# Kernel optimization log

Hardware: AMD Instinct MI355X
Metric: run time of the kernel (lower is better)

The kernel has to match this reference:

```python
import jax, jax.numpy as jnp
import numpy as np

T, B, IN, H = 1024, 128, 256, 512


def setup_inputs() -> dict:
    key = jax.random.key(0)
    k1, k2, k3, k4, k5 = jax.random.split(key, 5)
    s = 1.0 / np.sqrt(H)  # PyTorch LSTM init scale
    return {
        "x": jax.random.normal(k1, (T, B, IN), dtype=jnp.float32),
        "W_ih": jax.random.normal(k2, (4 * H, IN), dtype=jnp.float32) * s,
        "W_hh": jax.random.normal(k3, (4 * H, H), dtype=jnp.float32) * s,
        "b_ih": jax.random.normal(k4, (4 * H,), dtype=jnp.float32) * s,
        "b_hh": jax.random.normal(k5, (4 * H,), dtype=jnp.float32) * s,
    }


def reference(x, W_ih, W_hh, b_ih, b_hh):
    # Single-layer unidirectional LSTM scanned over the full sequence.
    # PyTorch gate order within the 4H dim: i, f, g, o.
    b = b_ih + b_hh
    Wx = jnp.einsum('tbi,gi->tbg', x, W_ih) + b  # precompute input projection [T,B,4H]

    def step(carry, zx):
        h, c = carry
        z = zx + h @ W_hh.T  # [B, 4H]
        i, f, g, o = jnp.split(z, 4, axis=-1)
        i = jax.nn.sigmoid(i)
        f = jax.nn.sigmoid(f)
        g = jnp.tanh(g)
        o = jax.nn.sigmoid(o)
        c = f * c + i * g
        h = o * jnp.tanh(c)
        return (h, c), None

    h0 = jnp.zeros((B, H), dtype=x.dtype)
    c0 = jnp.zeros((B, H), dtype=x.dtype)
    (h, c), _ = jax.lax.scan(step, (h0, c0), Wx)
    # Original returns the LAST step's output plus (h_n, c_n); with 1 layer output == h_n.
    output = h[None]          # [1, B, H]
    h_n = h[None]             # [num_layers=1, B, H]
    c_n = c[None]
    return (output, h_n, c_n)
```

## Files before the change

kernel.cpp:

```cpp
#include <hip/hip_runtime.h>
#include <hip/hip_bf16.h>

typedef __attribute__((ext_vector_type(8)))  short short8;
typedef __attribute__((ext_vector_type(16))) float f32x16;
typedef __attribute__((ext_vector_type(4)))  unsigned int uint4v;

#define TSTEPS 1024
#define BATCH  128
#define NIN    256
#define NHID   512
#define GM     4
#define MBLK   32
#define XPSTR  528
#define XBUF   8448
#define HSTR   520
#define HBUF   16640

__device__ __forceinline__ unsigned short f2bf(float f) {
  unsigned int u = __builtin_bit_cast(unsigned int, f);
  u += 0x7fffu + ((u >> 16) & 1u);
  return (unsigned short)(u >> 16);
}

__device__ __forceinline__ unsigned long long pack4(float a, float b, float c, float d) {
  return (unsigned long long)f2bf(a)
       | ((unsigned long long)f2bf(b) << 16)
       | ((unsigned long long)f2bf(c) << 32)
       | ((unsigned long long)f2bf(d) << 48);
}

__device__ __forceinline__ float sigf(float x) {
  return 1.0f / (1.0f + __expf(-x));
}
__device__ __forceinline__ float tanh_fast(float x) {
  x = fminf(fmaxf(x, -15.0f), 15.0f);
  float e = __expf(2.0f * x);
  return (e - 1.0f) / (e + 1.0f);
}

__global__ void init_ws_kernel(unsigned long long* hbuf, unsigned int* flags) {
  int idx = blockIdx.x * blockDim.x + threadIdx.x;
  if (idx < 16384) hbuf[idx] = 0ull;
  if (idx < 8192) flags[idx] = 0u;
}

__global__ void convert_x_kernel(const float* __restrict__ x, unsigned short* __restrict__ xbf) {
  const int N4 = TSTEPS * BATCH * NIN / 4;
  for (int i = blockIdx.x * blockDim.x + threadIdx.x; i < N4; i += gridDim.x * blockDim.x) {
    float4 f = *(const float4*)(x + (size_t)i * 4);
    *(unsigned long long*)(xbf + (size_t)i * 4) = pack4(f.x, f.y, f.z, f.w);
  }
}

#define MFMA(va, fb, acc) \
  acc = __builtin_amdgcn_mfma_f32_32x32x16_bf16(va, fb, acc, 0, 0, 0)

template <int USE_DMA>
__global__ __launch_bounds__(256, 1) void lstm_persistent(
    const float* __restrict__ x,
    const unsigned short* __restrict__ xbf,
    const float* __restrict__ Wih,
    const float* __restrict__ Whh,
    const float* __restrict__ bih,
    const float* __restrict__ bhh,
    float* __restrict__ out,
    unsigned long long* __restrict__ hbuf,
    unsigned int* __restrict__ flags)
{
  const int tid  = threadIdx.x;
  const int lane = tid & 63;
  const int wv   = tid >> 6;
  const int gm   = blockIdx.x & (GM - 1);
  const int gh   = blockIdx.x >> 2;
  const int m0   = gm * MBLK;
  const int hc0  = gh * 32;

  __shared__ short x_flat[3 * XBUF];
  __shared__ short h_flat[2 * HBUF];
  __shared__ float z_lds[4][MBLK][36];

  const int ncol = lane & 31;
  const int h5   = lane >> 5;
  const int arow = lane & 31;
  const int kg   = h5 * 8;
  const int gate = ncol >> 3;
  const int wrow = gate * NHID + hc0 + wv * 8 + (ncol & 7);

  short8 bfrag[48];
#pragma unroll
  for (int kb = 0; kb < 48; ++kb) {
    const float* src = (kb < 16)
        ? (Wih + (size_t)wrow * NIN  + (kb * 16 + kg))
        : (Whh + (size_t)wrow * NHID + (kb * 16 + kg - NIN));
    float4 f0 = *(const float4*)src;
    float4 f1 = *(const float4*)(src + 4);
    short8 b;
    b[0] = (short)f2bf(f0.x); b[1] = (short)f2bf(f0.y);
    b[2] = (short)f2bf(f0.z); b[3] = (short)f2bf(f0.w);
    b[4] = (short)f2bf(f1.x); b[5] = (short)f2bf(f1.y);
    b[6] = (short)f2bf(f1.z); b[7] = (short)f2bf(f1.w);
    bfrag[kb] = b;
  }
  const float bias_c = bih[wrow] + bhh[wrow];

  const int grow = tid >> 3;
  const int c4   = (tid & 7) * 4;
  float creg[4] = {0.0f, 0.0f, 0.0f, 0.0f};

  unsigned int* fgrp   = flags + gm * (64 * 32);
  unsigned int* myflag = fgrp + (gh * 4 + wv) * 32;

#define XLOAD(i, v) { int u = tid + 256 * (i); \
    v = *(const float4*)(xt + (size_t)(u >> 6) * NIN + (u & 63) * 4); }
#define XPACK(bb, i, v) { int u = tid + 256 * (i); int r = u >> 6; int hc = u & 63; \
    *(unsigned long long*)&x_flat[(bb) * XBUF + (r >> 1) * XPSTR + (r & 1) * NIN + hc * 4] \
        = pack4(v.x, v.y, v.z, v.w); }
#define XDMA(tt, bb) { \
    const unsigned short* gsrc = xbf + ((size_t)(tt) * BATCH + m0) * NIN; \
    short* ldst = x_flat + (bb) * XBUF; \
    _Pragma("unroll") \
    for (int j = 0; j < 4; ++j) { \
      int ck = 4 * wv + j; \
      const unsigned short* gp = gsrc + (size_t)(2 * ck + h5) * NIN + (lane & 31) * 8; \
      __builtin_amdgcn_global_load_lds((const unsigned int*)gp, \
          (unsigned int*)(ldst + ck * XPSTR), 16, 0, 0); \
    } }

  f32x16 a0, a1, a2, a3;
  float4 xv0, xv1, xv2, xv3, xv4, xv5, xv6, xv7;

  if (USE_DMA) {
    XDMA(0, 0) XDMA(1, 1) XDMA(2, 2)
    asm volatile("s_waitcnt vmcnt(0)" ::: "memory");
  } else {
    { const float* xt = x + (size_t)m0 * NIN;
      XLOAD(0, xv0) XLOAD(1, xv1) XLOAD(2, xv2) XLOAD(3, xv3)
      XLOAD(4, xv4) XLOAD(5, xv5) XLOAD(6, xv6) XLOAD(7, xv7)
      XPACK(0, 0, xv0) XPACK(0, 1, xv1) XPACK(0, 2, xv2) XPACK(0, 3, xv3)
      XPACK(0, 4, xv4) XPACK(0, 5, xv5) XPACK(0, 6, xv6) XPACK(0, 7, xv7) }
    { const float* xt = x + ((size_t)BATCH + m0) * NIN;
      XLOAD(0, xv0) XLOAD(1, xv1) XLOAD(2, xv2) XLOAD(3, xv3)
      XLOAD(4, xv4) XLOAD(5, xv5) XLOAD(6, xv6) XLOAD(7, xv7)
      XPACK(1, 0, xv0) XPACK(1, 1, xv1) XPACK(1, 2, xv2) XPACK(1, 3, xv3)
      XPACK(1, 4, xv4) XPACK(1, 5, xv5) XPACK(1, 6, xv6) XPACK(1, 7, xv7) }
  }
  __syncthreads();
  a0 = (f32x16)bias_c; a1 = (f32x16)0.0f; a2 = (f32x16)0.0f; a3 = (f32x16)0.0f;
  {
    const short* xrow = x_flat + (arow >> 1) * XPSTR + (arow & 1) * NIN + kg;
#pragma unroll
    for (int kb = 0; kb < 16; kb += 4) {
      MFMA(*(const short8*)(xrow + (kb + 0) * 16), bfrag[kb + 0], a0);
      MFMA(*(const short8*)(xrow + (kb + 1) * 16), bfrag[kb + 1], a1);
      MFMA(*(const short8*)(xrow + (kb + 2) * 16), bfrag[kb + 2], a2);
      MFMA(*(const short8*)(xrow + (kb + 3) * 16), bfrag[kb + 3], a3);
    }
  }

  int tmod = 0;
  for (int t = 0; t < TSTEPS; ++t) {
    if (t > 0) {
      const unsigned int* fp = fgrp + lane * 32;
      unsigned int v = __hip_atomic_load(fp, __ATOMIC_RELAXED, __HIP_MEMORY_SCOPE_AGENT);
      while (!__all((int)(v >= (unsigned int)t))) {
        v = __hip_atomic_load(fp, __ATOMIC_RELAXED, __HIP_MEMORY_SCOPE_AGENT);
      }
    }

    {
      const char* p =
          (const char*)(hbuf + (size_t)(t & 1) * 16384 + (size_t)m0 * 128) + tid * 16;
      uint4v hv0, hv1, hv2, hv3, hv4, hv5, hv6, hv7;
      asm volatile("global_load_dwordx4 %0, %1, off sc0 sc1" : "=v"(hv0) : "v"(p + 0 * 4096));
      asm volatile("global_load_dwordx4 %0, %1, off sc0 sc1" : "=v"(hv1) : "v"(p + 1 * 4096));
      asm volatile("global_load_dwordx4 %0, %1, off sc0 sc1" : "=v"(hv2) : "v"(p + 2 * 4096));
      asm volatile("global_load_dwordx4 %0, %1, off sc0 sc1" : "=v"(hv3) : "v"(p + 3 * 4096));
      asm volatile("global_load_dwordx4 %0, %1, off sc0 sc1" : "=v"(hv4) : "v"(p + 4 * 4096));
      asm volatile("global_load_dwordx4 %0, %1, off sc0 sc1" : "=v"(hv5) : "v"(p + 5 * 4096));
      asm volatile("global_load_dwordx4 %0, %1, off sc0 sc1" : "=v"(hv6) : "v"(p + 6 * 4096));
      asm volatile("global_load_dwordx4 %0, %1, off sc0 sc1" : "=v"(hv7) : "v"(p + 7 * 4096));
      asm volatile("s_waitcnt vmcnt(0)" ::: "memory");
      __builtin_amdgcn_sched_barrier(0);
      short* hdst = h_flat + (t & 1) * HBUF;
#pragma unroll
      for (int i = 0; i < 8; ++i) {
        int r = wv + 4 * i;
        uint4v v = (i == 0) ? hv0 : (i == 1) ? hv1 : (i == 2) ? hv2 : (i == 3) ? hv3
                 : (i == 4) ? hv4 : (i == 5) ? hv5 : (i == 6) ? hv6 : hv7;
        *(uint4v*)&hdst[r * HSTR + lane * 8] = v;
      }
    }
    __syncthreads();

    if (!USE_DMA && t + 2 < TSTEPS) {
      const float* xt = x + ((size_t)(t + 2) * BATCH + m0) * NIN;
      XLOAD(0, xv0) XLOAD(1, xv1) XLOAD(2, xv2) XLOAD(3, xv3)
      XLOAD(4, xv4) XLOAD(5, xv5) XLOAD(6, xv6) XLOAD(7, xv7)
    }

    {
      const short* hrow = h_flat + (t & 1) * HBUF + arow * HSTR + kg;
#pragma unroll
      for (int kb = 0; kb < 32; kb += 4) {
        MFMA(*(const short8*)(hrow + (kb + 0) * 16), bfrag[16 + kb + 0], a0);
        MFMA(*(const short8*)(hrow + (kb + 1) * 16), bfrag[16 + kb + 1], a1);
        MFMA(*(const short8*)(hrow + (kb + 2) * 16), bfrag[16 + kb + 2], a2);
        MFMA(*(const short8*)(hrow + (kb + 3) * 16), bfrag[16 + kb + 3], a3);
      }
    }

    {
      f32x16 acc = (a0 + a1) + (a2 + a3);
#pragma unroll
      for (int r = 0; r < 16; ++r) {
        int zr = (r & 3) + 8 * (r >> 2) + 4 * h5;
        z_lds[wv][zr][ncol] = acc[r];
      }
    }
    __syncthreads();

    {
      const int wz = c4 >> 3;
      const int cc = c4 & 7;
      const float* zrow = &z_lds[wz][grow][0];
      float4 vi = *(const float4*)&zrow[ 0 + cc];
      float4 vf = *(const float4*)&zrow[ 8 + cc];
      float4 vg = *(const float4*)&zrow[16 + cc];
      float4 vo = *(const float4*)&zrow[24 + cc];
      float zi[4] = {vi.x, vi.y, vi.z, vi.w};
      float zf[4] = {vf.x, vf.y, vf.z, vf.w};
      float zg[4] = {vg.x, vg.y, vg.z, vg.w};
      float zo[4] = {vo.x, vo.y, vo.z, vo.w};
      float hnv[4];
#pragma unroll
      for (int u = 0; u < 4; ++u) {
        float iv = sigf(zi[u]);
        float fv = sigf(zf[u]);
        float gv = tanh_fast(zg[u]);
        float ov = sigf(zo[u]);
        float cn = fv * creg[u] + iv * gv;
        creg[u] = cn;
        hnv[u] = ov * tanh_fast(cn);
      }
      if (t == TSTEPS - 1) {
        size_t o = (size_t)(m0 + grow) * NHID + hc0 + c4;
        float4 hq; hq.x = hnv[0]; hq.y = hnv[1]; hq.z = hnv[2]; hq.w = hnv[3];
        float4 cq; cq.x = creg[0]; cq.y = creg[1]; cq.z = creg[2]; cq.w = creg[3];
        *(float4*)&out[o]          = hq;
        *(float4*)&out[65536 + o]  = hq;
        *(float4*)&out[131072 + o] = cq;
      } else {
        unsigned long long hp = pack4(hnv[0], hnv[1], hnv[2], hnv[3]);
        size_t hoff = (size_t)((t + 1) & 1) * 16384
                    + (size_t)(m0 + grow) * 128 + (hc0 + c4) / 4;
        __hip_atomic_store(hbuf + hoff, hp, __ATOMIC_RELAXED, __HIP_MEMORY_SCOPE_AGENT);
        __builtin_amdgcn_sched_barrier(0);
        asm volatile("s_waitcnt vmcnt(0)" ::: "memory");
        if (lane == 0) {
          __hip_atomic_store(myflag, (unsigned int)(t + 1),
                             __ATOMIC_RELAXED, __HIP_MEMORY_SCOPE_AGENT);
        }
      }
    }

    if (t < TSTEPS - 1) {
      if (USE_DMA) {
        if (t + 3 < TSTEPS) { XDMA(t + 3, tmod) }
      } else if (t + 2 < TSTEPS) {
        int pb = tmod + 2; if (pb >= 3) pb -= 3;
        XPACK(pb, 0, xv0) XPACK(pb, 1, xv1) XPACK(pb, 2, xv2) XPACK(pb, 3, xv3)
        XPACK(pb, 4, xv4) XPACK(pb, 5, xv5) XPACK(pb, 6, xv6) XPACK(pb, 7, xv7)
      }
      int nb = tmod + 1; if (nb >= 3) nb -= 3;
      a0 = (f32x16)bias_c; a1 = (f32x16)0.0f; a2 = (f32x16)0.0f; a3 = (f32x16)0.0f;
      const short* xrow = x_flat + nb * XBUF + (arow >> 1) * XPSTR + (arow & 1) * NIN + kg;
#pragma unroll
      for (int kb = 0; kb < 16; kb += 4) {
        MFMA(*(const short8*)(xrow + (kb + 0) * 16), bfrag[kb + 0], a0);
        MFMA(*(const short8*)(xrow + (kb + 1) * 16), bfrag[kb + 1], a1);
        MFMA(*(const short8*)(xrow + (kb + 2) * 16), bfrag[kb + 2], a2);
        MFMA(*(const short8*)(xrow + (kb + 3) * 16), bfrag[kb + 3], a3);
      }
    }
    tmod = tmod + 1; if (tmod >= 3) tmod = 0;
  }
#undef XLOAD
#undef XPACK
#undef XDMA
}

extern "C" void kernel_launch(void* const* d_in, const int* in_sizes, int n_in,
                              void* d_out, int out_size, void* d_ws, size_t ws_size,
                              hipStream_t stream) {
  const float* x   = (const float*)d_in[0];
  const float* Wih = (const float*)d_in[1];
  const float* Whh = (const float*)d_in[2];
  const float* bih = (const float*)d_in[3];
  const float* bhh = (const float*)d_in[4];
  float* out = (float*)d_out;

  unsigned long long* hbuf = (unsigned long long*)d_ws;
  unsigned int* flags = (unsigned int*)((char*)d_ws + 262144);
  unsigned short* xbf = (unsigned short*)((char*)d_ws + (1 << 20));

  size_t need = (size_t)(1 << 20) + (size_t)TSTEPS * BATCH * NIN * 2;
  bool dma = ws_size >= need;

  hipLaunchKernelGGL(init_ws_kernel, dim3(64), dim3(256), 0, stream, hbuf, flags);
  if (dma) {
    hipLaunchKernelGGL(convert_x_kernel, dim3(8192), dim3(256), 0, stream, x, xbf);
    hipLaunchKernelGGL((lstm_persistent<1>), dim3(64), dim3(256), 0, stream,
                       x, xbf, Wih, Whh, bih, bhh, out, hbuf, flags);
  } else {
    hipLaunchKernelGGL((lstm_persistent<0>), dim3(64), dim3(256), 0, stream,
                       x, xbf, Wih, Whh, bih, bhh, out, hbuf, flags);
  }
}
```

Measured before the change: 3.565 ms.

## Embed step tags in hidden-state records to replace separate flag polling

Each 8-byte bf16 hidden-state chunk is now written as a 16-byte record with the timestep tag alongside it, in a single store. Consumers poll the records themselves until every tag matches the current step, which removes the separate flag spin-wait and the store-then-wait-then-flag round trip on the serial critical path. In exchange, it doubles the bytes moved per step for hidden-state exchange. It also relies on each 16-byte store being observed atomically, so data and tag arrive together.

```diff
diff --git a/kernel.cpp b/kernel.cpp
--- a/kernel.cpp
+++ b/kernel.cpp
@@ -38,10 +38,9 @@
   return (e - 1.0f) / (e + 1.0f);
 }
 
-__global__ void init_ws_kernel(unsigned long long* hbuf, unsigned int* flags) {
+__global__ void init_ws_kernel(unsigned long long* tbuf) {
   int idx = blockIdx.x * blockDim.x + threadIdx.x;
-  if (idx < 16384) hbuf[idx] = 0ull;
-  if (idx < 8192) flags[idx] = 0u;
+  for (int i = idx; i < 65536; i += 16384) tbuf[i] = 0ull;
 }
 
 __global__ void convert_x_kernel(const float* __restrict__ x, unsigned short* __restrict__ xbf) {
@@ -54,6 +53,9 @@
 
 #define MFMA(va, fb, acc) \
   acc = __builtin_amdgcn_mfma_f32_32x32x16_bf16(va, fb, acc, 0, 0, 0)
+
+#define CLOAD(cv, off) \
+  asm volatile("global_load_dwordx4 %0, %1, off sc0 sc1" : "=v"(cv) : "v"(rb + (off)))
 
 template <int USE_DMA>
 __global__ __launch_bounds__(256, 1) void lstm_persistent(
@@ -64,8 +66,7 @@
     const float* __restrict__ bih,
     const float* __restrict__ bhh,
     float* __restrict__ out,
-    unsigned long long* __restrict__ hbuf,
-    unsigned int* __restrict__ flags)
+    char* __restrict__ tbuf)
 {
   const int tid  = threadIdx.x;
   const int lane = tid & 63;
@@ -107,8 +108,8 @@
   const int c4   = (tid & 7) * 4;
   float creg[4] = {0.0f, 0.0f, 0.0f, 0.0f};
 
-  unsigned int* fgrp   = flags + gm * (64 * 32);
-  unsigned int* myflag = fgrp + (gh * 4 + wv) * 32;
+  const char* tb = tbuf + (size_t)gm * 131072;
+  const int  myci = grow * 128 + (hc0 >> 2) + (tid & 7);
 
 #define XLOAD(i, v) { int u = tid + 256 * (i); \
     v = *(const float4*)(xt + (size_t)(u >> 6) * NIN + (u & 63) * 4); }
@@ -159,36 +160,34 @@
 
   int tmod = 0;
   for (int t = 0; t < TSTEPS; ++t) {
-    if (t > 0) {
-      const unsigned int* fp = fgrp + lane * 32;
-      unsigned int v = __hip_atomic_load(fp, __ATOMIC_RELAXED, __HIP_MEMORY_SCOPE_AGENT);
-      while (!__all((int)(v >= (unsigned int)t))) {
-        v = __hip_atomic_load(fp, __ATOMIC_RELAXED, __HIP_MEMORY_SCOPE_AGENT);
-      }
-    }
-
     {
-      const char* p =
-          (const char*)(hbuf + (size_t)(t & 1) * 16384 + (size_t)m0 * 128) + tid * 16;
-      uint4v hv0, hv1, hv2, hv3, hv4, hv5, hv6, hv7;
-      asm volatile("global_load_dwordx4 %0, %1, off sc0 sc1" : "=v"(hv0) : "v"(p + 0 * 4096));
-      asm volatile("global_load_dwordx4 %0, %1, off sc0 sc1" : "=v"(hv1) : "v"(p + 1 * 4096));
-      asm volatile("global_load_dwordx4 %0, %1, off sc0 sc1" : "=v"(hv2) : "v"(p + 2 * 4096));
-      asm volatile("global_load_dwordx4 %0, %1, off sc0 sc1" : "=v"(hv3) : "v"(p + 3 * 4096));
-      asm volatile("global_load_dwordx4 %0, %1, off sc0 sc1" : "=v"(hv4) : "v"(p + 4 * 4096));
-      asm volatile("global_load_dwordx4 %0, %1, off sc0 sc1" : "=v"(hv5) : "v"(p + 5 * 4096));
-      asm volatile("global_load_dwordx4 %0, %1, off sc0 sc1" : "=v"(hv6) : "v"(p + 6 * 4096));
-      asm volatile("global_load_dwordx4 %0, %1, off sc0 sc1" : "=v"(hv7) : "v"(p + 7 * 4096));
-      asm volatile("s_waitcnt vmcnt(0)" ::: "memory");
+      const char* rb = tb + (size_t)(t & 1) * 65536 + (size_t)tid * 16;
+      const unsigned int tg = (unsigned int)t;
+      uint4v c0, c1, c2, c3, c4v, c5, c6, c7, c8, c9, c10, c11, c12, c13, c14, c15;
+      int ok;
+      do {
+        CLOAD(c0,  0 * 4096); CLOAD(c1,  1 * 4096); CLOAD(c2,  2 * 4096);
+        CLOAD(c3,  3 * 4096); CLOAD(c4v, 4 * 4096); CLOAD(c5,  5 * 4096);
+        CLOAD(c6,  6 * 4096); CLOAD(c7,  7 * 4096); CLOAD(c8,  8 * 4096);
+        CLOAD(c9,  9 * 4096); CLOAD(c10, 10 * 4096); CLOAD(c11, 11 * 4096);
+        CLOAD(c12, 12 * 4096); CLOAD(c13, 13 * 4096); CLOAD(c14, 14 * 4096);
+        CLOAD(c15, 15 * 4096);
+        asm volatile("s_waitcnt vmcnt(0)" ::: "memory");
+        ok = (c0.z == tg) & (c1.z == tg) & (c2.z == tg) & (c3.z == tg)
+           & (c4v.z == tg) & (c5.z == tg) & (c6.z == tg) & (c7.z == tg)
+           & (c8.z == tg) & (c9.z == tg) & (c10.z == tg) & (c11.z == tg)
+           & (c12.z == tg) & (c13.z == tg) & (c14.z == tg) & (c15.z == tg);
+      } while (!__all(ok));
       __builtin_amdgcn_sched_barrier(0);
       short* hdst = h_flat + (t & 1) * HBUF;
-#pragma unroll
-      for (int i = 0; i < 8; ++i) {
-        int r = wv + 4 * i;
-        uint4v v = (i == 0) ? hv0 : (i == 1) ? hv1 : (i == 2) ? hv2 : (i == 3) ? hv3
-                 : (i == 4) ? hv4 : (i == 5) ? hv5 : (i == 6) ? hv6 : hv7;
-        *(uint4v*)&hdst[r * HSTR + lane * 8] = v;
-      }
+#define HPUT(j, cv) { int ci = tid + 256 * (j); \
+      *(unsigned long long*)&hdst[(ci >> 7) * HSTR + (ci & 127) * 4] = \
+          (unsigned long long)cv.x | ((unsigned long long)cv.y << 32); }
+      HPUT(0, c0)  HPUT(1, c1)  HPUT(2, c2)  HPUT(3, c3)
+      HPUT(4, c4v) HPUT(5, c5)  HPUT(6, c6)  HPUT(7, c7)
+      HPUT(8, c8)  HPUT(9, c9)  HPUT(10, c10) HPUT(11, c11)
+      HPUT(12, c12) HPUT(13, c13) HPUT(14, c14) HPUT(15, c15)
+#undef HPUT
     }
     __syncthreads();
 
@@ -251,15 +250,14 @@
         *(float4*)&out[131072 + o] = cq;
       } else {
         unsigned long long hp = pack4(hnv[0], hnv[1], hnv[2], hnv[3]);
-        size_t hoff = (size_t)((t + 1) & 1) * 16384
-                    + (size_t)(m0 + grow) * 128 + (hc0 + c4) / 4;
-        __hip_atomic_store(hbuf + hoff, hp, __ATOMIC_RELAXED, __HIP_MEMORY_SCOPE_AGENT);
-        __builtin_amdgcn_sched_barrier(0);
-        asm volatile("s_waitcnt vmcnt(0)" ::: "memory");
-        if (lane == 0) {
-          __hip_atomic_store(myflag, (unsigned int)(t + 1),
-                             __ATOMIC_RELAXED, __HIP_MEMORY_SCOPE_AGENT);
-        }
+        uint4v sv;
+        sv.x = (unsigned int)hp;
+        sv.y = (unsigned int)(hp >> 32);
+        sv.z = (unsigned int)(t + 1);
+        sv.w = 0u;
+        const char* wb = tb + (size_t)((t + 1) & 1) * 65536 + (size_t)myci * 16;
+        asm volatile("global_store_dwordx4 %0, %1, off sc0 sc1"
+                     :: "v"(wb), "v"(sv) : "memory");
       }
     }
 
@@ -299,20 +297,20 @@
   const float* bhh = (const float*)d_in[4];
   float* out = (float*)d_out;
 
-  unsigned long long* hbuf = (unsigned long long*)d_ws;
-  unsigned int* flags = (unsigned int*)((char*)d_ws + 262144);
+  char* tbuf = (char*)d_ws;
   unsigned short* xbf = (unsigned short*)((char*)d_ws + (1 << 20));
 
   size_t need = (size_t)(1 << 20) + (size_t)TSTEPS * BATCH * NIN * 2;
   bool dma = ws_size >= need;
 
-  hipLaunchKernelGGL(init_ws_kernel, dim3(64), dim3(256), 0, stream, hbuf, flags);
+  hipLaunchKernelGGL(init_ws_kernel, dim3(64), dim3(256), 0, stream,
+                     (unsigned long long*)tbuf);
   if (dma) {
     hipLaunchKernelGGL(convert_x_kernel, dim3(8192), dim3(256), 0, stream, x, xbf);
     hipLaunchKernelGGL((lstm_persistent<1>), dim3(64), dim3(256), 0, stream,
-                       x, xbf, Wih, Whh, bih, bhh, out, hbuf, flags);
+                       x, xbf, Wih, Whh, bih, bhh, out, tbuf);
   } else {
     hipLaunchKernelGGL((lstm_persistent<0>), dim3(64), dim3(256), 0, stream,
-                       x, xbf, Wih, Whh, bih, bhh, out, hbuf, flags);
-  }
-}
+                       x, xbf, Wih, Whh, bih, bhh, out, tbuf);
+  }
+}
```

Result: faster. 3.392 ms (-4.9%).
